# Kernel tuning notes

Measured on AMD Instinct MI355X. Metric: run time of the kernel, lower is better.

## Reference

```python
import jax, jax.numpy as jnp
import numpy as np

B, M, C, D, FF, FEAT = 1, 1024, 128, 512, 1024, 20
PAIR = 3 * D + 2 * FEAT  # slow_scorer_size = 1576


def _ffnn(x, W0, b0, W1, b1):
    # FFNN(depth=1): hidden relu layer then linear output (eval mode, no dropout)
    return jax.nn.relu(x @ W0 + b0) @ W1 + b1


def _batch_gather(x, idx):
    # x: [B, M, ...], idx: [B, ...] int -> gather along mention dim per batch
    return jax.vmap(lambda xb, ib: xb[ib])(x, idx)


def _bucket_distance(d):
    # log-scale distance buckets 0..9 (identity for d<=4)
    log_idx = jnp.floor(jnp.log(jnp.maximum(d, 1).astype(jnp.float32)) / jnp.log(2.0)).astype(jnp.int32) + 3
    return jnp.clip(jnp.where(d <= 4, d, log_idx), 0, 9)


def setup_inputs() -> dict:
    key = jax.random.key(0)
    ks = jax.random.split(key, 10)
    s = 0.02
    return {
        'mention_emb': jax.random.normal(ks[0], (B, M, D), dtype=jnp.float32),
        'mention_cluster_ids': jax.random.randint(ks[1], (B, M), 0, 200),
        'mention_speaker_ids': jax.random.randint(ks[2], (B, M), 0, 2),
        'ms_W0': jax.random.normal(ks[3], (D, FF), dtype=jnp.float32) * s,
        'ms_b0': jnp.zeros((FF,), jnp.float32),
        'ms_W1': jax.random.normal(ks[4], (FF, 1), dtype=jnp.float32) * s,
        'ms_b1': jnp.zeros((1,), jnp.float32),
        'sp_W0': jax.random.normal(ks[5], (PAIR, FF), dtype=jnp.float32) * s,
        'sp_b0': jnp.zeros((FF,), jnp.float32),
        'sp_W1': jax.random.normal(ks[6], (FF, 1), dtype=jnp.float32) * s,
        'sp_b1': jnp.zeros((1,), jnp.float32),
        'speaker_emb': jax.random.normal(ks[7], (2, FEAT), dtype=jnp.float32) * s,
        'bucket_emb': jax.random.normal(ks[8], (10, FEAT), dtype=jnp.float32) * s,
    }


def reference(mention_emb, mention_cluster_ids, mention_speaker_ids,
              ms_W0, ms_b0, ms_W1, ms_b1,
              sp_W0, sp_b0, sp_W1, sp_b1,
              speaker_emb, bucket_emb):
    # mention scoring
    mention_scores = _ffnn(mention_emb, ms_W0, ms_b0, ms_W1, ms_b1)[..., 0]  # [B, M]

    # get_antecedent_info: fixed window of C previous mentions
    offsets = jnp.arange(1, C + 1)[None, None, :]                    # [1,1,C]
    raw = jnp.arange(M)[None, :, None] - offsets                      # [1,M,C]
    antecedents = jnp.broadcast_to(jnp.clip(raw, 0, M - 1), (B, M, C))
    ant_mask = jnp.broadcast_to(raw >= 0, (B, M, C))

    fast_scores = _batch_gather(mention_scores, antecedents) + mention_scores[:, :, None]
    antecedent_emb = _batch_gather(mention_emb, antecedents)          # [B,M,C,D]

    # slow pair scorer features
    same_speaker = (_batch_gather(mention_speaker_ids, antecedents) == mention_speaker_ids[:, :, None]).astype(jnp.int32)
    speaker_feat = speaker_emb[same_speaker]                          # [B,M,C,FEAT]
    bucket_feat = jnp.broadcast_to(bucket_emb[_bucket_distance(offsets)], (B, M, C, FEAT))

    src = jnp.broadcast_to(mention_emb[:, :, None, :], (B, M, C, D))
    pair_emb = jnp.concatenate([src, antecedent_emb, src * antecedent_emb, speaker_feat, bucket_feat], axis=-1)
    slow_scores = _ffnn(pair_emb, sp_W0, sp_b0, sp_W1, sp_b1)[..., 0]  # [B,M,C]

    antecedent_scores = fast_scores + slow_scores + jnp.log(ant_mask.astype(jnp.float32))
    overall_scores = jnp.concatenate([jnp.zeros((B, M, 1), jnp.float32), antecedent_scores], axis=2)
    overall_dist = jax.nn.softmax(overall_scores, axis=-1)
    eps = 1e-6
    overall_dist = jnp.clip(overall_dist, eps, 1.0 - eps)
    overall_dist = overall_dist / jnp.sum(overall_dist, axis=-1, keepdims=True)

    # coref loss from cluster ids
    ant_cluster = _batch_gather(mention_cluster_ids, antecedents) * ant_mask.astype(mention_cluster_ids.dtype)
    same_cluster = ant_cluster == mention_cluster_ids[:, :, None]
    non_dummy = (mention_cluster_ids > 0)[:, :, None]
    ant_labels = same_cluster & non_dummy
    dummy_labels = ~jnp.any(ant_labels, axis=2, keepdims=True)
    overall_labels = jnp.concatenate([dummy_labels, ant_labels], axis=2)
    loss = -jnp.sum(jnp.log(overall_dist) * overall_labels.astype(jnp.float32), axis=2)
    loss = jnp.mean(jnp.sum(loss, axis=1))
    return overall_dist, loss
```

## Files before the change

kernel.cpp:

```cpp
#include <hip/hip_runtime.h>
#include <math.h>

#define MM 1024
#define DD 512
#define CC 128
#define LDSR 516


typedef __attribute__((ext_vector_type(8))) short bf16x8;
typedef __attribute__((ext_vector_type(4), aligned(8))) short bf16x4a;
typedef __attribute__((ext_vector_type(4))) float f32x4;
typedef __attribute__((ext_vector_type(16))) float f32x16;

__device__ __forceinline__ ushort bf16_rn(float x) {
    uint u = __float_as_uint(x);
    uint r = u + 0x7fffu + ((u >> 16) & 1u);
    return (ushort)(r >> 16);
}
__device__ __forceinline__ float bf16_to_f(ushort u) {
    return __uint_as_float(((uint)u) << 16);
}
__device__ __forceinline__ bf16x8 ld_lds16(const ushort* p) {
    bf16x4a lo = *(const bf16x4a*)p;
    bf16x4a hi = *(const bf16x4a*)(p + 4);
    return __builtin_shufflevector(lo, hi, 0, 1, 2, 3, 4, 5, 6, 7);
}

__global__ __launch_bounds__(256) void prep_emb(const float* __restrict__ emb,
                                                ushort* __restrict__ embb)
{
    int i = blockIdx.x * 256 + threadIdx.x;
    float2 v = ((const float2*)emb)[i];
    ushort2 o;
    o.x = bf16_rn(v.x);
    o.y = bf16_rn(v.y);
    ((ushort2*)embb)[i] = o;
}

__global__ __launch_bounds__(256) void prep_wall(const float* __restrict__ ms_W0,
                                                 const float* __restrict__ sp_W0,
                                                 ushort* __restrict__ Wall)
{
    __shared__ float t[64][65];
    const int k0 = blockIdx.x * 64;
    const int n0 = blockIdx.y * 64;
    const int g = n0 >> 10;
    const float* src = (g == 0) ? ms_W0 : (sp_W0 + (size_t)(g - 1) * 512 * 1024);
    const int col0 = n0 & 1023;
    const int tr = threadIdx.x >> 6, tc = threadIdx.x & 63;
#pragma unroll
    for (int i = 0; i < 16; ++i) {
        int k = tr + i * 4;
        t[k][tc] = src[(size_t)(k0 + k) * 1024 + col0 + tc];
    }
    __syncthreads();
    const int f = threadIdx.x >> 2;
    const int c4 = threadIdx.x & 3;
    ushort tmp[16];
#pragma unroll
    for (int j = 0; j < 16; ++j) tmp[j] = bf16_rn(t[c4 * 16 + j][f]);
    uint4* dst = (uint4*)(Wall + (size_t)(n0 + f) * 512 + k0 + c4 * 16);
    dst[0] = *(uint4*)&tmp[0];
    dst[1] = *(uint4*)&tmp[8];
}

__global__ __launch_bounds__(64) void prep_wfrag(const float* __restrict__ sp_W0,
                                                 ushort* __restrict__ Wfrag)
{
    const int ts = blockIdx.x;
    const int l = threadIdx.x;
    const int tt = ts >> 5, s = ts & 31;
    const int f = tt * 32 + (l & 31);
    const int kb = s * 16 + (l >> 5) * 8;
    const float* W = sp_W0 + (size_t)1024 * 1024;
    ushort tmp[8];
#pragma unroll
    for (int j = 0; j < 8; ++j) tmp[j] = bf16_rn(W[(size_t)(kb + j) * 1024 + f]);
    uint4* dst = (uint4*)(Wfrag + ((size_t)ts * 64 + l) * 8);
    *dst = *(uint4*)&tmp[0];
}

__global__ __launch_bounds__(256) void gemm_h_mfma(
    const ushort* __restrict__ embb, const ushort* __restrict__ Wall,
    float* __restrict__ H2, ushort* __restrict__ antb)
{
    const int n0 = blockIdx.x * 128;
    const int m0 = blockIdx.y * 128;
    const int lane = threadIdx.x & 63, wave = threadIdx.x >> 6;
    const int wx = wave & 1, wy = wave >> 1;
    const int l15 = lane & 15, lq = lane >> 4;

    const ushort* arow[4];
#pragma unroll
    for (int mi = 0; mi < 4; ++mi)
        arow[mi] = embb + (size_t)(m0 + wy * 64 + mi * 16 + l15) * 512;
    const ushort* brow[4];
#pragma unroll
    for (int ni = 0; ni < 4; ++ni)
        brow[ni] = Wall + (size_t)(n0 + wx * 64 + ni * 16 + l15) * 512;

    f32x4 acc[4][4];
#pragma unroll
    for (int i = 0; i < 4; ++i)
#pragma unroll
        for (int j = 0; j < 4; ++j) acc[i][j] = (f32x4)0.f;

    for (int kt = 0; kt < 512; kt += 32) {
        const int ko = kt + lq * 8;
        bf16x8 av[4], bv[4];
#pragma unroll
        for (int mi = 0; mi < 4; ++mi) av[mi] = *(const bf16x8*)(arow[mi] + ko);
#pragma unroll
        for (int ni = 0; ni < 4; ++ni) bv[ni] = *(const bf16x8*)(brow[ni] + ko);
#pragma unroll
        for (int mi = 0; mi < 4; ++mi)
#pragma unroll
            for (int ni = 0; ni < 4; ++ni)
                acc[mi][ni] = __builtin_amdgcn_mfma_f32_16x16x32_bf16(av[mi], bv[ni], acc[mi][ni], 0, 0, 0);
    }
    if (n0 < 2048) {
#pragma unroll
        for (int mi = 0; mi < 4; ++mi)
#pragma unroll
            for (int r = 0; r < 4; ++r) {
                int mrow = m0 + wy * 64 + mi * 16 + lq * 4 + r;
#pragma unroll
                for (int ni = 0; ni < 4; ++ni)
                    H2[(size_t)mrow * 2048 + n0 + wx * 64 + ni * 16 + l15] = acc[mi][ni][r];
            }
    } else {
#pragma unroll
        for (int mi = 0; mi < 4; ++mi)
#pragma unroll
            for (int r = 0; r < 4; ++r) {
                int mrow = m0 + wy * 64 + mi * 16 + lq * 4 + r;
#pragma unroll
                for (int ni = 0; ni < 4; ++ni)
                    antb[(size_t)mrow * 1024 + (n0 - 2048) + wx * 64 + ni * 16 + l15] =
                        bf16_rn(acc[mi][ni][r]);
            }
    }
}

__global__ void small_proj(const float* __restrict__ speaker_emb,
                           const float* __restrict__ bucket_emb,
                           const float* __restrict__ sp_W0,
                           float* __restrict__ spk_proj, float* __restrict__ bkt_proj)
{
    int r = blockIdx.x;
    const float* e; const float* W; float* out;
    if (r < 2) { e = speaker_emb + r * 20; W = sp_W0 + (size_t)1536 * 1024; out = spk_proj + r * 1024; }
    else       { e = bucket_emb + (r - 2) * 20; W = sp_W0 + (size_t)1556 * 1024; out = bkt_proj + (r - 2) * 1024; }
    float ek[20];
#pragma unroll
    for (int k = 0; k < 20; ++k) ek[k] = e[k];
    for (int f = threadIdx.x; f < 1024; f += blockDim.x) {
        float s = 0.f;
#pragma unroll
        for (int k = 0; k < 20; ++k) s = fmaf(ek[k], W[(size_t)k * 1024 + f], s);
        out[f] = s;
    }
}

__global__ __launch_bounds__(256) void mention_score(
    const float* __restrict__ H2, const float* __restrict__ ms_b0,
    const float* __restrict__ ms_W1, const float* __restrict__ ms_b1,
    float* __restrict__ ms)
{
    int m = blockIdx.x;
    float v = 0.f;
    for (int f = threadIdx.x; f < 1024; f += 256) {
        float h = H2[(size_t)m * 2048 + f] + ms_b0[f];
        v += fmaxf(h, 0.f) * ms_W1[f];
    }
#pragma unroll
    for (int o = 1; o < 64; o <<= 1) v += __shfl_xor(v, o);
    __shared__ float sm[4];
    if ((threadIdx.x & 63) == 0) sm[threadIdx.x >> 6] = v;
    __syncthreads();
    if (threadIdx.x == 0) ms[m] = sm[0] + sm[1] + sm[2] + sm[3] + ms_b1[0];
}

__global__ __launch_bounds__(1024, 4) void pair_mfma(
    const ushort* __restrict__ embb, const ushort* __restrict__ Wfrag,
    const float* __restrict__ H2, const ushort* __restrict__ antb,
    const float* __restrict__ spk_proj, const float* __restrict__ bkt_proj,
    const float* __restrict__ sp_b0, const float* __restrict__ sp_W1,
    const int* __restrict__ speaker, float* __restrict__ slow)
{
    extern __shared__ ushort Alds[];
    float* red = (float*)(Alds + 128 * LDSR);
    int* meta_ss = (int*)(red + 16 * 128);
    int* meta_bk = meta_ss + 128;
    const int m = blockIdx.x;
    const int tid = threadIdx.x;
    const int spk_m = speaker[m];

    {
        const int c = tid & 127;
        const int kh = (tid >> 7) * 64;
        int a = m - 1 - c; if (a < 0) a = 0;
        const ushort* ea = embb + (size_t)a * 512 + kh;
        const ushort* em = embb + (size_t)m * 512 + kh;
        ushort* dst = Alds + c * LDSR + kh;
#pragma unroll
        for (int j = 0; j < 64; j += 8) {
            bf16x8 va = *(const bf16x8*)(ea + j);
            bf16x8 vm = *(const bf16x8*)(em + j);
            uint pr[4];
#pragma unroll
            for (int p = 0; p < 4; ++p) {
                float q0 = bf16_to_f((ushort)va[2 * p])     * bf16_to_f((ushort)vm[2 * p]);
                float q1 = bf16_to_f((ushort)va[2 * p + 1]) * bf16_to_f((ushort)vm[2 * p + 1]);
                pr[p] = __builtin_amdgcn_perm(__float_as_uint(q1), __float_as_uint(q0), 0x07060302u);
            }
            *(uint2*)(dst + j)     = *(uint2*)&pr[0];
            *(uint2*)(dst + j + 4) = *(uint2*)&pr[2];
        }
        if (tid < 128) {
            const int cc = tid;
            int aa = m - 1 - cc; if (aa < 0) aa = 0;
            meta_ss[cc] = (speaker[aa] == spk_m) ? 1 : 0;
            int off = cc + 1;
            int bk;
            if (off <= 4) bk = off;
            else { bk = 31 - __clz(off) + 3; if (bk > 9) bk = 9; }
            meta_bk[cc] = bk;
        }
    }
    __syncthreads();

    const int lane = tid & 63;
    const int wave = __builtin_amdgcn_readfirstlane(tid >> 6);
    const int l31 = lane & 31, k5 = lane >> 5;
    const int f0 = wave * 64;
    const int srot = (wave >> 2) * 8;

    const ushort* bb = Wfrag + (size_t)(wave * 2) * 16384 + (size_t)lane * 8;
    const ushort* ab = Alds + l31 * LDSR + k5 * 8;

    for (int pass = 0; pass < 2; ++pass) {
        const int c0 = pass * 64;
        const ushort* ap = ab + c0 * LDSR;
        f32x16 acc[2][2];
#pragma unroll
        for (int i = 0; i < 2; ++i)
#pragma unroll
            for (int j = 0; j < 2; ++j) acc[i][j] = (f32x16)0.f;

        bf16x8 av[2][2], bv[2][2];
#pragma unroll
        for (int p = 0; p < 2; ++p) {
            const int ss = (p + srot) & 31;
            bv[p][0] = *(const bf16x8*)(bb + ss * 512);
            bv[p][1] = *(const bf16x8*)(bb + 16384 + ss * 512);
            av[p][0] = ld_lds16(ap + ss * 16);
            av[p][1] = ld_lds16(ap + 32 * LDSR + ss * 16);
        }
#pragma unroll 2
        for (int i = 0; i < 32; ++i) {
            const int cur = i & 1;
            acc[0][0] = __builtin_amdgcn_mfma_f32_32x32x16_bf16(av[cur][0], bv[cur][0], acc[0][0], 0, 0, 0);
            acc[0][1] = __builtin_amdgcn_mfma_f32_32x32x16_bf16(av[cur][0], bv[cur][1], acc[0][1], 0, 0, 0);
            acc[1][0] = __builtin_amdgcn_mfma_f32_32x32x16_bf16(av[cur][1], bv[cur][0], acc[1][0], 0, 0, 0);
            acc[1][1] = __builtin_amdgcn_mfma_f32_32x32x16_bf16(av[cur][1], bv[cur][1], acc[1][1], 0, 0, 0);
            const int ss = (i + 2 + srot) & 31;
            bv[cur][0] = *(const bf16x8*)(bb + ss * 512);
            bv[cur][1] = *(const bf16x8*)(bb + 16384 + ss * 512);
            av[cur][0] = ld_lds16(ap + ss * 16);
            av[cur][1] = ld_lds16(ap + 32 * LDSR + ss * 16);
        }

        float srcb[2], w1v[2], sp0v[2], sp1v[2], bk9v[2];
#pragma unroll
        for (int ni = 0; ni < 2; ++ni) {
            int fcol = f0 + ni * 32 + l31;
            srcb[ni] = H2[(size_t)m * 2048 + 1024 + fcol] + sp_b0[fcol];
            w1v[ni]  = sp_W1[fcol];
            sp0v[ni] = spk_proj[fcol];
            sp1v[ni] = spk_proj[1024 + fcol];
            bk9v[ni] = bkt_proj[9 * 1024 + fcol];
        }
#pragma unroll
        for (int mi = 0; mi < 2; ++mi) {
#pragma unroll
            for (int reg = 0; reg < 16; ++reg) {
                const int c = c0 + mi * 32 + 4 * k5 + (reg & 3) + 8 * (reg >> 2);
                int a = m - 1 - c; if (a < 0) a = 0;
                const int ss2 = meta_ss[c];
                const ushort* antp = antb + (size_t)a * 1024;
                float s = 0.f;
#pragma unroll
                for (int ni = 0; ni < 2; ++ni) {
                    const int fcol = f0 + ni * 32 + l31;
                    float bval = pass ? bk9v[ni] : bkt_proj[(size_t)meta_bk[c] * 1024 + fcol];
                    float antv = bf16_to_f(antp[fcol]);
                    float pre = acc[mi][ni][reg] + srcb[ni] + antv + (ss2 ? sp1v[ni] : sp0v[ni]) + bval;
                    s += fmaxf(pre, 0.f) * w1v[ni];
                }
                s += __shfl_xor(s, 1); s += __shfl_xor(s, 2); s += __shfl_xor(s, 4);
                s += __shfl_xor(s, 8); s += __shfl_xor(s, 16);
                if (l31 == 0) red[wave * 128 + c] = s;
            }
        }
    }
    __syncthreads();
    if (tid < 128) {
        float s = 0.f;
#pragma unroll
        for (int i = 0; i < 16; ++i) s += red[i * 128 + tid];
        slow[(size_t)m * 128 + tid] = s;
    }
}

__device__ __forceinline__ float bsum2(float v, float* sm) {
#pragma unroll
    for (int o = 1; o < 64; o <<= 1) v += __shfl_xor(v, o);
    __syncthreads();
    if ((threadIdx.x & 63) == 0) sm[threadIdx.x >> 6] = v;
    __syncthreads();
    return sm[0] + sm[1];
}
__device__ __forceinline__ float bmax2(float v, float* sm) {
#pragma unroll
    for (int o = 1; o < 64; o <<= 1) v = fmaxf(v, __shfl_xor(v, o));
    __syncthreads();
    if ((threadIdx.x & 63) == 0) sm[threadIdx.x >> 6] = v;
    __syncthreads();
    return fmaxf(sm[0], sm[1]);
}

__global__ __launch_bounds__(128) void softmax_loss(
    const float* __restrict__ slow, const float* __restrict__ ms,
    const float* __restrict__ sp_b1, const int* __restrict__ cluster,
    float* __restrict__ out, float* __restrict__ loss_partial)
{
    const int m = blockIdx.x, c = threadIdx.x;
    __shared__ float sm[2];
    const int raw = m - 1 - c;
    const bool maskv = raw >= 0;
    const int a = maskv ? raw : 0;
    float score = slow[(size_t)m * 128 + c] + sp_b1[0] + ms[m] + ms[a];
    if (!maskv) score = -INFINITY;

    float mx = fmaxf(bmax2(score, sm), 0.f);
    float e = expf(score - mx);
    float e0 = expf(0.f - mx);
    float sum = bsum2(e, sm) + e0;
    float p = e / sum, p0 = e0 / sum;
    const float eps = 1e-6f;
    p  = fminf(fmaxf(p,  eps), 1.f - eps);
    p0 = fminf(fmaxf(p0, eps), 1.f - eps);
    float sum2 = bsum2(p, sm) + p0;
    p /= sum2; p0 /= sum2;
    out[(size_t)m * 129 + 1 + c] = p;
    if (c == 0) out[(size_t)m * 129] = p0;

    const int cid = cluster[m];
    const bool lbl = maskv && (cid > 0) && (cluster[a] == cid);
    float anyc = bsum2(lbl ? 1.f : 0.f, sm);
    float lsum = bsum2(lbl ? -logf(p) : 0.f, sm);
    if (c == 0) {
        if (anyc == 0.f) lsum += -logf(p0);
        loss_partial[m] = lsum;
    }
}

__global__ void loss_sum(const float* __restrict__ lp, float* __restrict__ out) {
    float v = 0.f;
    for (int i = threadIdx.x; i < 1024; i += 256) v += lp[i];
#pragma unroll
    for (int o = 1; o < 64; o <<= 1) v += __shfl_xor(v, o);
    __shared__ float sm[4];
    if ((threadIdx.x & 63) == 0) sm[threadIdx.x >> 6] = v;
    __syncthreads();
    if (threadIdx.x == 0) out[(size_t)1024 * 129] = sm[0] + sm[1] + sm[2] + sm[3];
}

extern "C" void kernel_launch(void* const* d_in, const int* in_sizes, int n_in,
                              void* d_out, int out_size, void* d_ws, size_t ws_size,
                              hipStream_t stream)
{
    const float* emb   = (const float*)d_in[0];
    const int*   clus  = (const int*)  d_in[1];
    const int*   spk   = (const int*)  d_in[2];
    const float* ms_W0 = (const float*)d_in[3];
    const float* ms_b0 = (const float*)d_in[4];
    const float* ms_W1 = (const float*)d_in[5];
    const float* ms_b1 = (const float*)d_in[6];
    const float* sp_W0 = (const float*)d_in[7];
    const float* sp_b0 = (const float*)d_in[8];
    const float* sp_W1 = (const float*)d_in[9];
    const float* sp_b1 = (const float*)d_in[10];
    const float* spke  = (const float*)d_in[11];
    const float* bkte  = (const float*)d_in[12];

    float* ws = (float*)d_ws;
    float*  H2       = ws;
    ushort* antb     = (ushort*)(ws + 2097152);
    float*  slow     = ws + 2621440;
    float*  spk_proj = ws + 2752512;
    float*  bkt_proj = ws + 2754560;
    float*  msc      = ws + 2764800;
    float*  lossp    = ws + 2765824;
    ushort* embb     = (ushort*)(ws + 2766848);
    ushort* Wall     = (ushort*)(ws + 3028992);
    ushort* Wfrag    = Wall + (size_t)3072 * 512;
    float* out = (float*)d_out;

    const int pair_lds = 128 * LDSR * 2 + 16 * 128 * 4 + 256 * 4;

    static bool attr_set = false;
    if (!attr_set) {
        hipFuncSetAttribute((const void*)pair_mfma,
                            hipFuncAttributeMaxDynamicSharedMemorySize,
                            pair_lds);
        attr_set = true;
    }

    hipLaunchKernelGGL(prep_emb, dim3(1024), dim3(256), 0, stream, emb, embb);
    hipLaunchKernelGGL(prep_wall, dim3(8, 48), dim3(256), 0, stream, ms_W0, sp_W0, Wall);
    hipLaunchKernelGGL(prep_wfrag, dim3(1024), dim3(64), 0, stream, sp_W0, Wfrag);
    hipLaunchKernelGGL(gemm_h_mfma, dim3(24, 8), dim3(256), 0, stream, embb, Wall, H2, antb);
    hipLaunchKernelGGL(small_proj, dim3(12), dim3(256), 0, stream, spke, bkte, sp_W0, spk_proj, bkt_proj);
    hipLaunchKernelGGL(mention_score, dim3(1024), dim3(256), 0, stream, H2, ms_b0, ms_W1, ms_b1, msc);
    hipLaunchKernelGGL(pair_mfma, dim3(1024), dim3(1024), pair_lds, stream,
                       embb, Wfrag, H2, antb, spk_proj, bkt_proj, sp_b0, sp_W1, spk, slow);
    hipLaunchKernelGGL(softmax_loss, dim3(1024), dim3(128), 0, stream,
                       slow, msc, sp_b1, clus, out, lossp);
    hipLaunchKernelGGL(loss_sum, dim3(1), dim3(256), 0, stream, lossp, out);
}
```

Measured before the change: 390.7 us.

## Re-tile pair_mfma waves over antecedent×feature grid with register-held epilogue reduction

The 16 waves are re-split into 4 antecedent groups × 4 feature groups. Each wave now handles 32 antecedents across 256 features in four feature-tile passes instead of all 128 antecedents across 64 features. The relu·W1 products are accumulated in registers across the passes, so the shuffle reduction runs once and the LDS reduction buffer and final sum shrink. This cuts the repeated epilogue shuffles and the per-wave weight fragment traffic, in exchange for more loads from the A tile in LDS and a different prefetch pattern for the weights.

```diff
diff --git a/kernel.cpp b/kernel.cpp
--- a/kernel.cpp
+++ b/kernel.cpp
@@ -190,7 +190,7 @@
 {
     extern __shared__ ushort Alds[];
     float* red = (float*)(Alds + 128 * LDSR);
-    int* meta_ss = (int*)(red + 16 * 128);
+    int* meta_ss = (int*)(red + 512);
     int* meta_bk = meta_ss + 128;
     const int m = blockIdx.x;
     const int tid = threadIdx.x;
@@ -232,84 +232,100 @@
 
     const int lane = tid & 63;
     const int wave = __builtin_amdgcn_readfirstlane(tid >> 6);
+    const int wc = wave & 3;
+    const int wf = wave >> 2;
     const int l31 = lane & 31, k5 = lane >> 5;
-    const int f0 = wave * 64;
-    const int srot = (wave >> 2) * 8;
-
-    const ushort* bb = Wfrag + (size_t)(wave * 2) * 16384 + (size_t)lane * 8;
-    const ushort* ab = Alds + l31 * LDSR + k5 * 8;
-
-    for (int pass = 0; pass < 2; ++pass) {
-        const int c0 = pass * 64;
-        const ushort* ap = ab + c0 * LDSR;
-        f32x16 acc[2][2];
-#pragma unroll
-        for (int i = 0; i < 2; ++i)
-#pragma unroll
-            for (int j = 0; j < 2; ++j) acc[i][j] = (f32x16)0.f;
-
-        bf16x8 av[2][2], bv[2][2];
-#pragma unroll
-        for (int p = 0; p < 2; ++p) {
-            const int ss = (p + srot) & 31;
-            bv[p][0] = *(const bf16x8*)(bb + ss * 512);
-            bv[p][1] = *(const bf16x8*)(bb + 16384 + ss * 512);
-            av[p][0] = ld_lds16(ap + ss * 16);
-            av[p][1] = ld_lds16(ap + 32 * LDSR + ss * 16);
-        }
-#pragma unroll 2
-        for (int i = 0; i < 32; ++i) {
-            const int cur = i & 1;
-            acc[0][0] = __builtin_amdgcn_mfma_f32_32x32x16_bf16(av[cur][0], bv[cur][0], acc[0][0], 0, 0, 0);
-            acc[0][1] = __builtin_amdgcn_mfma_f32_32x32x16_bf16(av[cur][0], bv[cur][1], acc[0][1], 0, 0, 0);
-            acc[1][0] = __builtin_amdgcn_mfma_f32_32x32x16_bf16(av[cur][1], bv[cur][0], acc[1][0], 0, 0, 0);
-            acc[1][1] = __builtin_amdgcn_mfma_f32_32x32x16_bf16(av[cur][1], bv[cur][1], acc[1][1], 0, 0, 0);
-            const int ss = (i + 2 + srot) & 31;
-            bv[cur][0] = *(const bf16x8*)(bb + ss * 512);
-            bv[cur][1] = *(const bf16x8*)(bb + 16384 + ss * 512);
-            av[cur][0] = ld_lds16(ap + ss * 16);
-            av[cur][1] = ld_lds16(ap + 32 * LDSR + ss * 16);
-        }
-
-        float srcb[2], w1v[2], sp0v[2], sp1v[2], bk9v[2];
-#pragma unroll
-        for (int ni = 0; ni < 2; ++ni) {
-            int fcol = f0 + ni * 32 + l31;
-            srcb[ni] = H2[(size_t)m * 2048 + 1024 + fcol] + sp_b0[fcol];
-            w1v[ni]  = sp_W1[fcol];
-            sp0v[ni] = spk_proj[fcol];
-            sp1v[ni] = spk_proj[1024 + fcol];
-            bk9v[ni] = bkt_proj[9 * 1024 + fcol];
-        }
-#pragma unroll
-        for (int mi = 0; mi < 2; ++mi) {
-#pragma unroll
-            for (int reg = 0; reg < 16; ++reg) {
-                const int c = c0 + mi * 32 + 4 * k5 + (reg & 3) + 8 * (reg >> 2);
-                int a = m - 1 - c; if (a < 0) a = 0;
-                const int ss2 = meta_ss[c];
-                const ushort* antp = antb + (size_t)a * 1024;
-                float s = 0.f;
-#pragma unroll
-                for (int ni = 0; ni < 2; ++ni) {
-                    const int fcol = f0 + ni * 32 + l31;
-                    float bval = pass ? bk9v[ni] : bkt_proj[(size_t)meta_bk[c] * 1024 + fcol];
-                    float antv = bf16_to_f(antp[fcol]);
-                    float pre = acc[mi][ni][reg] + srcb[ni] + antv + (ss2 ? sp1v[ni] : sp0v[ni]) + bval;
-                    s += fmaxf(pre, 0.f) * w1v[ni];
-                }
-                s += __shfl_xor(s, 1); s += __shfl_xor(s, 2); s += __shfl_xor(s, 4);
-                s += __shfl_xor(s, 8); s += __shfl_xor(s, 16);
-                if (l31 == 0) red[wave * 128 + c] = s;
+
+    const ushort* ap = Alds + (size_t)(wc * 32 + l31) * LDSR + k5 * 8;
+    const ushort* wbase = Wfrag + (size_t)lane * 8;
+
+    float racc[16];
+#pragma unroll
+    for (int r = 0; r < 16; ++r) racc[r] = 0.f;
+
+    bf16x8 av[4], b0[4], b1[4];
+    {
+        const ushort* B0 = wbase + (size_t)(wf * 8 + 0) * 16384;
+        const ushort* B1 = wbase + (size_t)(wf * 8 + 1) * 16384;
+#pragma unroll
+        for (int j = 0; j < 4; ++j) {
+            av[j] = ld_lds16(ap + j * 16);
+            b0[j] = *(const bf16x8*)(B0 + j * 512);
+            b1[j] = *(const bf16x8*)(B1 + j * 512);
+        }
+    }
+
+    for (int ftp = 0; ftp < 4; ++ftp) {
+        f32x16 acc0 = (f32x16)0.f, acc1 = (f32x16)0.f;
+        const ushort* B0 = wbase + (size_t)(wf * 8 + ftp * 2) * 16384 + 4 * 512;
+        const ushort* B1 = B0 + 16384;
+        const int ntp = (ftp + 1) & 3;
+        const ushort* B0n = wbase + (size_t)(wf * 8 + ntp * 2) * 16384;
+        const ushort* B1n = B0n + 16384;
+
+        for (int g = 0; g < 7; ++g) {
+#pragma unroll
+            for (int j = 0; j < 4; ++j) {
+                acc0 = __builtin_amdgcn_mfma_f32_32x32x16_bf16(av[j], b0[j], acc0, 0, 0, 0);
+                acc1 = __builtin_amdgcn_mfma_f32_32x32x16_bf16(av[j], b1[j], acc1, 0, 0, 0);
             }
-        }
+            const int aoff = (g + 1) * 64;
+#pragma unroll
+            for (int j = 0; j < 4; ++j) {
+                av[j] = ld_lds16(ap + aoff + j * 16);
+                b0[j] = *(const bf16x8*)(B0 + j * 512);
+                b1[j] = *(const bf16x8*)(B1 + j * 512);
+            }
+            B0 += 4 * 512; B1 += 4 * 512;
+        }
+#pragma unroll
+        for (int j = 0; j < 4; ++j) {
+            acc0 = __builtin_amdgcn_mfma_f32_32x32x16_bf16(av[j], b0[j], acc0, 0, 0, 0);
+            acc1 = __builtin_amdgcn_mfma_f32_32x32x16_bf16(av[j], b1[j], acc1, 0, 0, 0);
+        }
+#pragma unroll
+        for (int j = 0; j < 4; ++j) {
+            av[j] = ld_lds16(ap + j * 16);
+            b0[j] = *(const bf16x8*)(B0n + j * 512);
+            b1[j] = *(const bf16x8*)(B1n + j * 512);
+        }
+
+        const int fcol0 = (wf * 8 + ftp * 2) * 32 + l31;
+        const int fcol1 = fcol0 + 32;
+        float srcb0 = H2[(size_t)m * 2048 + 1024 + fcol0] + sp_b0[fcol0];
+        float srcb1 = H2[(size_t)m * 2048 + 1024 + fcol1] + sp_b0[fcol1];
+        float w1v0 = sp_W1[fcol0], w1v1 = sp_W1[fcol1];
+        float sp00 = spk_proj[fcol0], sp01 = spk_proj[1024 + fcol0];
+        float sp10 = spk_proj[fcol1], sp11 = spk_proj[1024 + fcol1];
+#pragma unroll
+        for (int reg = 0; reg < 16; ++reg) {
+            const int c = wc * 32 + 4 * k5 + (reg & 3) + 8 * (reg >> 2);
+            int a = m - 1 - c; if (a < 0) a = 0;
+            const int ss2 = meta_ss[c];
+            const int bk = meta_bk[c];
+            float ant0 = bf16_to_f(antb[(size_t)a * 1024 + fcol0]);
+            float ant1 = bf16_to_f(antb[(size_t)a * 1024 + fcol1]);
+            float bv0 = bkt_proj[(size_t)bk * 1024 + fcol0];
+            float bv1 = bkt_proj[(size_t)bk * 1024 + fcol1];
+            float pre0 = acc0[reg] + srcb0 + ant0 + (ss2 ? sp01 : sp00) + bv0;
+            float pre1 = acc1[reg] + srcb1 + ant1 + (ss2 ? sp11 : sp10) + bv1;
+            racc[reg] += fmaxf(pre0, 0.f) * w1v0 + fmaxf(pre1, 0.f) * w1v1;
+        }
+    }
+
+#pragma unroll
+    for (int reg = 0; reg < 16; ++reg) {
+        float s = racc[reg];
+        s += __shfl_xor(s, 1); s += __shfl_xor(s, 2); s += __shfl_xor(s, 4);
+        s += __shfl_xor(s, 8); s += __shfl_xor(s, 16);
+        if (l31 == 0) red[wave * 32 + 4 * k5 + (reg & 3) + 8 * (reg >> 2)] = s;
     }
     __syncthreads();
     if (tid < 128) {
-        float s = 0.f;
-#pragma unroll
-        for (int i = 0; i < 16; ++i) s += red[i * 128 + tid];
-        slow[(size_t)m * 128 + tid] = s;
+        const int c = tid, wcc = c >> 5, cl = c & 31;
+        float s = red[(0 * 4 + wcc) * 32 + cl] + red[(1 * 4 + wcc) * 32 + cl]
+                + red[(2 * 4 + wcc) * 32 + cl] + red[(3 * 4 + wcc) * 32 + cl];
+        slow[(size_t)m * 128 + c] = s;
     }
 }
 
@@ -408,7 +424,7 @@
     ushort* Wfrag    = Wall + (size_t)3072 * 512;
     float* out = (float*)d_out;
 
-    const int pair_lds = 128 * LDSR * 2 + 16 * 128 * 4 + 256 * 4;
+    const int pair_lds = 128 * LDSR * 2 + 512 * 4 + 256 * 4;
 
     static bool attr_set = false;
     if (!attr_set) {
```

Measured after the change: 1.182 ms. +202.7%, slower.

## Split pair kernel per antecedent half with fragment-ordered LDS and weight layouts

Applied to the files above, without the earlier changes.

The pair-scoring kernel now runs 2x1024 blocks of 512 threads, each handling 64 antecedents instead of 128. The A operand is written to LDS already in MFMA fragment order, so each lane reads one 16-byte vector instead of two 8-byte halves. The weights are repacked so each wave covers 32 rows by 128 features with four accumulators. This is meant to raise occupancy and cut LDS read cost. The price is that each weight fragment is loaded from global memory twice as often across blocks, and each block loads embeddings with a different access pattern.

```diff
diff --git a/kernel.cpp b/kernel.cpp
--- a/kernel.cpp
+++ b/kernel.cpp
@@ -4,11 +4,9 @@
 #define MM 1024
 #define DD 512
 #define CC 128
-#define LDSR 516
 
 
 typedef __attribute__((ext_vector_type(8))) short bf16x8;
-typedef __attribute__((ext_vector_type(4), aligned(8))) short bf16x4a;
 typedef __attribute__((ext_vector_type(4))) float f32x4;
 typedef __attribute__((ext_vector_type(16))) float f32x16;
 
@@ -19,11 +17,6 @@
 }
 __device__ __forceinline__ float bf16_to_f(ushort u) {
     return __uint_as_float(((uint)u) << 16);
-}
-__device__ __forceinline__ bf16x8 ld_lds16(const ushort* p) {
-    bf16x4a lo = *(const bf16x4a*)p;
-    bf16x4a hi = *(const bf16x4a*)(p + 4);
-    return __builtin_shufflevector(lo, hi, 0, 1, 2, 3, 4, 5, 6, 7);
 }
 
 __global__ __launch_bounds__(256) void prep_emb(const float* __restrict__ emb,
@@ -64,19 +57,20 @@
     dst[1] = *(uint4*)&tmp[8];
 }
 
-__global__ __launch_bounds__(64) void prep_wfrag(const float* __restrict__ sp_W0,
-                                                 ushort* __restrict__ Wfrag)
-{
-    const int ts = blockIdx.x;
-    const int l = threadIdx.x;
-    const int tt = ts >> 5, s = ts & 31;
-    const int f = tt * 32 + (l & 31);
+__global__ __launch_bounds__(256) void prep_wfrag2(const float* __restrict__ sp_W0,
+                                                   ushort* __restrict__ Wfrag2)
+{
+    const int g = blockIdx.x;
+    const int s = blockIdx.y;
+    const int t = threadIdx.x >> 6;
+    const int l = threadIdx.x & 63;
+    const int f = g * 128 + t * 32 + (l & 31);
     const int kb = s * 16 + (l >> 5) * 8;
     const float* W = sp_W0 + (size_t)1024 * 1024;
     ushort tmp[8];
 #pragma unroll
     for (int j = 0; j < 8; ++j) tmp[j] = bf16_rn(W[(size_t)(kb + j) * 1024 + f]);
-    uint4* dst = (uint4*)(Wfrag + ((size_t)ts * 64 + l) * 8);
+    uint4* dst = (uint4*)(Wfrag2 + ((((size_t)g * 32 + s) * 4 + t) * 64 + l) * 8);
     *dst = *(uint4*)&tmp[0];
 }
 
@@ -181,32 +175,34 @@
     if (threadIdx.x == 0) ms[m] = sm[0] + sm[1] + sm[2] + sm[3] + ms_b1[0];
 }
 
-__global__ __launch_bounds__(1024, 4) void pair_mfma(
-    const ushort* __restrict__ embb, const ushort* __restrict__ Wfrag,
+__global__ __launch_bounds__(512, 4) void pair_mfma(
+    const ushort* __restrict__ embb, const ushort* __restrict__ Wfrag2,
     const float* __restrict__ H2, const ushort* __restrict__ antb,
     const float* __restrict__ spk_proj, const float* __restrict__ bkt_proj,
     const float* __restrict__ sp_b0, const float* __restrict__ sp_W1,
     const int* __restrict__ speaker, float* __restrict__ slow)
 {
-    extern __shared__ ushort Alds[];
-    float* red = (float*)(Alds + 128 * LDSR);
-    int* meta_ss = (int*)(red + 16 * 128);
-    int* meta_bk = meta_ss + 128;
-    const int m = blockIdx.x;
+    extern __shared__ ushort Afrag[];
+    float* red = (float*)(Afrag + 32768);
+    int* meta_ss = (int*)(red + 512);
+    int* meta_bk = meta_ss + 64;
+    const int ch = blockIdx.x;
+    const int m = blockIdx.y;
     const int tid = threadIdx.x;
     const int spk_m = speaker[m];
 
     {
-        const int c = tid & 127;
-        const int kh = (tid >> 7) * 64;
-        int a = m - 1 - c; if (a < 0) a = 0;
-        const ushort* ea = embb + (size_t)a * 512 + kh;
-        const ushort* em = embb + (size_t)m * 512 + kh;
-        ushort* dst = Alds + c * LDSR + kh;
-#pragma unroll
-        for (int j = 0; j < 64; j += 8) {
-            bf16x8 va = *(const bf16x8*)(ea + j);
-            bf16x8 vm = *(const bf16x8*)(em + j);
+        const int c = tid >> 3;
+        const int q = tid & 7;
+        const int cg = ch * 64 + c;
+        int a = m - 1 - cg; if (a < 0) a = 0;
+        const ushort* ea = embb + (size_t)a * 512 + q * 64;
+        const ushort* em = embb + (size_t)m * 512 + q * 64;
+        const int ct = c >> 5, c31 = c & 31;
+#pragma unroll
+        for (int j0 = 0; j0 < 64; j0 += 8) {
+            bf16x8 va = *(const bf16x8*)(ea + j0);
+            bf16x8 vm = *(const bf16x8*)(em + j0);
             uint pr[4];
 #pragma unroll
             for (int p = 0; p < 4; ++p) {
@@ -214,14 +210,15 @@
                 float q1 = bf16_to_f((ushort)va[2 * p + 1]) * bf16_to_f((ushort)vm[2 * p + 1]);
                 pr[p] = __builtin_amdgcn_perm(__float_as_uint(q1), __float_as_uint(q0), 0x07060302u);
             }
-            *(uint2*)(dst + j)     = *(uint2*)&pr[0];
-            *(uint2*)(dst + j + 4) = *(uint2*)&pr[2];
+            const int s = q * 4 + (j0 >> 4);
+            const int h = (j0 >> 3) & 1;
+            ((uint4*)Afrag)[(ct * 32 + s) * 64 + h * 32 + c31] = *(uint4*)pr;
         }
-        if (tid < 128) {
-            const int cc = tid;
-            int aa = m - 1 - cc; if (aa < 0) aa = 0;
+        if (tid < 64) {
+            const int cc = tid, cgg = ch * 64 + cc;
+            int aa = m - 1 - cgg; if (aa < 0) aa = 0;
             meta_ss[cc] = (speaker[aa] == spk_m) ? 1 : 0;
-            int off = cc + 1;
+            int off = cgg + 1;
             int bk;
             if (off <= 4) bk = off;
             else { bk = 31 - __clz(off) + 3; if (bk > 9) bk = 9; }
@@ -232,84 +229,93 @@
 
     const int lane = tid & 63;
     const int wave = __builtin_amdgcn_readfirstlane(tid >> 6);
+    const int wc = wave & 1;
+    const int wf = wave >> 1;
     const int l31 = lane & 31, k5 = lane >> 5;
-    const int f0 = wave * 64;
-    const int srot = (wave >> 2) * 8;
-
-    const ushort* bb = Wfrag + (size_t)(wave * 2) * 16384 + (size_t)lane * 8;
-    const ushort* ab = Alds + l31 * LDSR + k5 * 8;
+
+    const ushort* ap = Afrag + ((size_t)wc * 2048 + lane) * 8;
 
     for (int pass = 0; pass < 2; ++pass) {
-        const int c0 = pass * 64;
-        const ushort* ap = ab + c0 * LDSR;
-        f32x16 acc[2][2];
-#pragma unroll
-        for (int i = 0; i < 2; ++i)
-#pragma unroll
-            for (int j = 0; j < 2; ++j) acc[i][j] = (f32x16)0.f;
-
-        bf16x8 av[2][2], bv[2][2];
-#pragma unroll
-        for (int p = 0; p < 2; ++p) {
-            const int ss = (p + srot) & 31;
-            bv[p][0] = *(const bf16x8*)(bb + ss * 512);
-            bv[p][1] = *(const bf16x8*)(bb + 16384 + ss * 512);
-            av[p][0] = ld_lds16(ap + ss * 16);
-            av[p][1] = ld_lds16(ap + 32 * LDSR + ss * 16);
+        const int g = pass * 4 + wf;
+        const ushort* P  = Wfrag2 + (size_t)g * 65536 + (size_t)lane * 8;
+        const ushort* P2 = P + 2048;
+
+        f32x16 acc0 = (f32x16)0.f, acc1 = (f32x16)0.f;
+        f32x16 acc2 = (f32x16)0.f, acc3 = (f32x16)0.f;
+        bf16x8 a[2], b[2][4];
+
+        a[0] = *(const bf16x8*)(ap);
+        a[1] = *(const bf16x8*)(ap + 512);
+        b[0][0] = *(const bf16x8*)(P);
+        b[0][1] = *(const bf16x8*)(P + 1024);
+        b[0][2] = *(const bf16x8*)(P2);
+        b[0][3] = *(const bf16x8*)(P2 + 1024);
+        P += 2048; P2 += 2048;
+        b[1][0] = *(const bf16x8*)(P);
+        b[1][1] = *(const bf16x8*)(P + 1024);
+        b[1][2] = *(const bf16x8*)(P2);
+        b[1][3] = *(const bf16x8*)(P2 + 1024);
+        P += 2048; P2 += 2048;
+
+#pragma unroll
+        for (int s = 0; s < 32; ++s) {
+            const int cur = s & 1;
+            acc0 = __builtin_amdgcn_mfma_f32_32x32x16_bf16(a[cur], b[cur][0], acc0, 0, 0, 0);
+            acc1 = __builtin_amdgcn_mfma_f32_32x32x16_bf16(a[cur], b[cur][1], acc1, 0, 0, 0);
+            acc2 = __builtin_amdgcn_mfma_f32_32x32x16_bf16(a[cur], b[cur][2], acc2, 0, 0, 0);
+            acc3 = __builtin_amdgcn_mfma_f32_32x32x16_bf16(a[cur], b[cur][3], acc3, 0, 0, 0);
+            a[cur] = *(const bf16x8*)(ap + (s + 2) * 512);
+            b[cur][0] = *(const bf16x8*)(P);
+            b[cur][1] = *(const bf16x8*)(P + 1024);
+            b[cur][2] = *(const bf16x8*)(P2);
+            b[cur][3] = *(const bf16x8*)(P2 + 1024);
+            P += 2048; P2 += 2048;
         }
-#pragma unroll 2
-        for (int i = 0; i < 32; ++i) {
-            const int cur = i & 1;
-            acc[0][0] = __builtin_amdgcn_mfma_f32_32x32x16_bf16(av[cur][0], bv[cur][0], acc[0][0], 0, 0, 0);
-            acc[0][1] = __builtin_amdgcn_mfma_f32_32x32x16_bf16(av[cur][0], bv[cur][1], acc[0][1], 0, 0, 0);
-            acc[1][0] = __builtin_amdgcn_mfma_f32_32x32x16_bf16(av[cur][1], bv[cur][0], acc[1][0], 0, 0, 0);
-            acc[1][1] = __builtin_amdgcn_mfma_f32_32x32x16_bf16(av[cur][1], bv[cur][1], acc[1][1], 0, 0, 0);
-            const int ss = (i + 2 + srot) & 31;
-            bv[cur][0] = *(const bf16x8*)(bb + ss * 512);
-            bv[cur][1] = *(const bf16x8*)(bb + 16384 + ss * 512);
-            av[cur][0] = ld_lds16(ap + ss * 16);
-            av[cur][1] = ld_lds16(ap + 32 * LDSR + ss * 16);
+
+        const int fb = g * 128 + l31;
+        float srcb[4], w1v[4], sp0v[4], sp1v[4];
+#pragma unroll
+        for (int t = 0; t < 4; ++t) {
+            const int fcol = fb + t * 32;
+            srcb[t] = H2[(size_t)m * 2048 + 1024 + fcol] + sp_b0[fcol];
+            w1v[t]  = sp_W1[fcol];
+            sp0v[t] = spk_proj[fcol];
+            sp1v[t] = spk_proj[1024 + fcol];
         }
-
-        float srcb[2], w1v[2], sp0v[2], sp1v[2], bk9v[2];
-#pragma unroll
-        for (int ni = 0; ni < 2; ++ni) {
-            int fcol = f0 + ni * 32 + l31;
-            srcb[ni] = H2[(size_t)m * 2048 + 1024 + fcol] + sp_b0[fcol];
-            w1v[ni]  = sp_W1[fcol];
-            sp0v[ni] = spk_proj[fcol];
-            sp1v[ni] = spk_proj[1024 + fcol];
-            bk9v[ni] = bkt_proj[9 * 1024 + fcol];
+#pragma unroll
+        for (int reg = 0; reg < 16; ++reg) {
+            const int row = 4 * k5 + (reg & 3) + 8 * (reg >> 2);
+            const int c = wc * 32 + row;
+            const int cg = ch * 64 + c;
+            int a2 = m - 1 - cg; if (a2 < 0) a2 = 0;
+            const int ss2 = meta_ss[c];
+            const int bk = meta_bk[c];
+            const ushort* antp = antb + (size_t)a2 * 1024;
+            const float* bkp = bkt_proj + (size_t)bk * 1024;
+            float s = 0.f;
+            float av4[4] = { acc0[reg], acc1[reg], acc2[reg], acc3[reg] };
+#pragma unroll
+            for (int t = 0; t < 4; ++t) {
+                const int fcol = fb + t * 32;
+                float pre = av4[t] + srcb[t] + bf16_to_f(antp[fcol])
+                          + (ss2 ? sp1v[t] : sp0v[t]) + bkp[fcol];
+                s += fmaxf(pre, 0.f) * w1v[t];
+            }
+            s += __shfl_xor(s, 1); s += __shfl_xor(s, 2); s += __shfl_xor(s, 4);
+            s += __shfl_xor(s, 8); s += __shfl_xor(s, 16);
+            if (l31 == 0) red[pass * 256 + wave * 32 + row] = s;
         }
-#pragma unroll
-        for (int mi = 0; mi < 2; ++mi) {
-#pragma unroll
-            for (int reg = 0; reg < 16; ++reg) {
-                const int c = c0 + mi * 32 + 4 * k5 + (reg & 3) + 8 * (reg >> 2);
-                int a = m - 1 - c; if (a < 0) a = 0;
-                const int ss2 = meta_ss[c];
-                const ushort* antp = antb + (size_t)a * 1024;
-                float s = 0.f;
-#pragma unroll
-                for (int ni = 0; ni < 2; ++ni) {
-                    const int fcol = f0 + ni * 32 + l31;
-                    float bval = pass ? bk9v[ni] : bkt_proj[(size_t)meta_bk[c] * 1024 + fcol];
-                    float antv = bf16_to_f(antp[fcol]);
-                    float pre = acc[mi][ni][reg] + srcb[ni] + antv + (ss2 ? sp1v[ni] : sp0v[ni]) + bval;
-                    s += fmaxf(pre, 0.f) * w1v[ni];
-                }
-                s += __shfl_xor(s, 1); s += __shfl_xor(s, 2); s += __shfl_xor(s, 4);
-                s += __shfl_xor(s, 8); s += __shfl_xor(s, 16);
-                if (l31 == 0) red[wave * 128 + c] = s;
-            }
-        }
-    }
-    __syncthreads();
-    if (tid < 128) {
+    }
+    __syncthreads();
+    if (tid < 64) {
+        const int c = tid, row = c & 31, wcc = c >> 5;
         float s = 0.f;
 #pragma unroll
-        for (int i = 0; i < 16; ++i) s += red[i * 128 + tid];
-        slow[(size_t)m * 128 + tid] = s;
+        for (int pass = 0; pass < 2; ++pass)
+#pragma unroll
+            for (int wff = 0; wff < 4; ++wff)
+                s += red[pass * 256 + (wff * 2 + wcc) * 32 + row];
+        slow[(size_t)m * 128 + ch * 64 + c] = s;
     }
 }
 
@@ -405,10 +411,10 @@
     float*  lossp    = ws + 2765824;
     ushort* embb     = (ushort*)(ws + 2766848);
     ushort* Wall     = (ushort*)(ws + 3028992);
-    ushort* Wfrag    = Wall + (size_t)3072 * 512;
+    ushort* Wfrag2   = Wall + (size_t)3072 * 512;
     float* out = (float*)d_out;
 
-    const int pair_lds = 128 * LDSR * 2 + 16 * 128 * 4 + 256 * 4;
+    const int pair_lds = 32768 * 2 + 512 * 4 + 128 * 4;
 
     static bool attr_set = false;
     if (!attr_set) {
@@ -420,12 +426,12 @@
 
     hipLaunchKernelGGL(prep_emb, dim3(1024), dim3(256), 0, stream, emb, embb);
     hipLaunchKernelGGL(prep_wall, dim3(8, 48), dim3(256), 0, stream, ms_W0, sp_W0, Wall);
-    hipLaunchKernelGGL(prep_wfrag, dim3(1024), dim3(64), 0, stream, sp_W0, Wfrag);
+    hipLaunchKernelGGL(prep_wfrag2, dim3(8, 32), dim3(256), 0, stream, sp_W0, Wfrag2);
     hipLaunchKernelGGL(gemm_h_mfma, dim3(24, 8), dim3(256), 0, stream, embb, Wall, H2, antb);
     hipLaunchKernelGGL(small_proj, dim3(12), dim3(256), 0, stream, spke, bkte, sp_W0, spk_proj, bkt_proj);
     hipLaunchKernelGGL(mention_score, dim3(1024), dim3(256), 0, stream, H2, ms_b0, ms_W1, ms_b1, msc);
-    hipLaunchKernelGGL(pair_mfma, dim3(1024), dim3(1024), pair_lds, stream,
-                       embb, Wfrag, H2, antb, spk_proj, bkt_proj, sp_b0, sp_W1, spk, slow);
+    hipLaunchKernelGGL(pair_mfma, dim3(2, 1024), dim3(512), pair_lds, stream,
+                       embb, Wfrag2, H2, antb, spk_proj, bkt_proj, sp_b0, sp_W1, spk, slow);
     hipLaunchKernelGGL(softmax_loss, dim3(1024), dim3(128), 0, stream,
                        slow, msc, sp_b1, clus, out, lossp);
     hipLaunchKernelGGL(loss_sum, dim3(1), dim3(256), 0, stream, lossp, out);
```

After: 466.4 us. 1.19x slower.
